# Optimization experiments

Hardware: AMD Instinct MI355X
Metric: run time of the kernel (lower is better)

The kernel has to match this reference:

```python
import jax, jax.numpy as jnp
import numpy as np

DIM = 192
HEADS = 6
HIDDEN = 384  # int(dim * mlp_ratio)


def conv2d(x, w, b=None, padding=0, groups=1):
    out = jax.lax.conv_general_dilated(
        x, w, (1, 1), [(padding, padding), (padding, padding)],
        feature_group_count=groups,
        dimension_numbers=('NCHW', 'OIHW', 'NCHW'))
    return out if b is None else out + b[None, :, None, None]


def layernorm(x, g, b, eps=1e-5):
    m = x.mean(-1, keepdims=True)
    v = x.var(-1, keepdims=True)  # biased, matches torch LayerNorm
    return (x - m) / jnp.sqrt(v + eps) * g + b


def l2norm(x, eps=1e-12):  # F.normalize(dim=-1)
    n = jnp.linalg.norm(x, axis=-1, keepdims=True)
    return x / jnp.maximum(n, eps)


def setup_inputs() -> dict:
    key = jax.random.key(0)
    ks = jax.random.split(key, 12)
    s = 0.02
    return {
        'x': jax.random.normal(ks[0], (4, DIM, 128, 128), dtype=jnp.float32),
        'g1': jnp.ones((DIM,), jnp.float32),
        'b1': jnp.zeros((DIM,), jnp.float32),
        'w_qkv': jax.random.normal(ks[1], (3 * DIM, DIM, 1, 1), jnp.float32) * s,
        'w_dw': jax.random.normal(ks[2], (3 * DIM, 1, 3, 3), jnp.float32) * s,
        'temp': jnp.ones((HEADS, 1, 1), jnp.float32),
        'w_head': jax.random.normal(ks[3], (HEADS, HEADS, 3, 3), jnp.float32) * s,
        'w_proj': jax.random.normal(ks[4], (DIM, DIM, 1, 1), jnp.float32) * s,
        'g2': jnp.ones((DIM,), jnp.float32),
        'b2': jnp.zeros((DIM,), jnp.float32),
        'w_fc1': jax.random.normal(ks[5], (HIDDEN, DIM), jnp.float32) * s,
        'b_fc1': jnp.zeros((HIDDEN,), jnp.float32),
        'w_fc2': jax.random.normal(ks[6], (DIM, HIDDEN), jnp.float32) * s,
        'b_fc2': jnp.zeros((DIM,), jnp.float32),
        'w_sa': jax.random.normal(ks[7], (1, DIM, 3, 3), jnp.float32) * s,
        'b_sa': jnp.zeros((1,), jnp.float32),
    }


def reference(x, g1, b1, w_qkv, w_dw, temp, w_head, w_proj, g2, b2,
              w_fc1, b_fc1, w_fc2, b_fc2, w_sa, b_sa):
    b, c, h, w = x.shape
    hw = h * w
    # norm1 (note: original code re-assigns x, so residual uses normed x)
    xf = x.reshape(b, c, hw).transpose(0, 2, 1)          # [b, hw, c]
    x1 = layernorm(xf, g1, b1).transpose(0, 2, 1).reshape(b, c, h, w)
    # channel attention (Restormer style)
    qkv = conv2d(conv2d(x1, w_qkv), w_dw, padding=1, groups=3 * c)
    q, k, v = jnp.split(qkv, 3, axis=1)
    cp = c // HEADS
    q = l2norm(q.reshape(b, HEADS, cp, hw))
    k = l2norm(k.reshape(b, HEADS, cp, hw))
    v = v.reshape(b, HEADS, cp, hw)
    attn = jnp.einsum('bhcn,bhdn->bhcd', q, k) * temp    # [b, heads, cp, cp]
    attn = conv2d(attn, w_head, padding=1)               # conv over head channels
    attn = jax.nn.softmax(attn, axis=-1)
    out = jnp.einsum('bhcd,bhdn->bhcn', attn, v).reshape(b, c, h, w)
    out = conv2d(out, w_proj)
    x2 = x1 + out
    # MLP branch with spatial-gating attn
    x3 = x2.reshape(b, c, hw).transpose(0, 2, 1)         # [b, hw, c]
    y = layernorm(x3, g2, b2)
    y = jax.nn.gelu(y @ w_fc1.T + b_fc1, approximate=False)
    y = y @ w_fc2.T + b_fc2
    y = jax.nn.gelu(y, approximate=False)                # SAAttn act_fn
    y4 = y.reshape(b, h, w, c).transpose(0, 3, 1, 2)     # [b, c, h, w]
    gate = jax.nn.sigmoid(conv2d(y4, w_sa, b_sa, padding=1))  # [b,1,h,w]
    y = (y4 * gate).reshape(b, c, hw).transpose(0, 2, 1)
    x4 = x3 + y
    return x4.transpose(0, 2, 1).reshape(b, c, h, w)
```

## Files before the change

kernel.cpp:

```cpp
#include <hip/hip_runtime.h>
#include <hip/hip_bf16.h>
#include <math.h>

using bf16 = __hip_bfloat16;

static constexpr int CDIM   = 192;
static constexpr int HEADS  = 6;
static constexpr int CP     = 32;
static constexpr int HIDDEN = 384;
static constexpr int HImg   = 128;
static constexpr int WImg   = 128;
static constexpr int HW     = HImg * WImg;
static constexpr int BATCH  = 4;
static constexpr int PCHUNK = 256;
static constexpr int CSPLIT = 12;

typedef __attribute__((ext_vector_type(8))) short short8;
typedef __attribute__((ext_vector_type(4))) float f32x4;
typedef __attribute__((ext_vector_type(4))) unsigned short ushort4v;
typedef __attribute__((ext_vector_type(8))) unsigned short ushort8v;

template<typename T> __device__ inline float tof(T v);
template<> __device__ inline float tof<float>(float v){ return v; }
template<> __device__ inline float tof<bf16>(bf16 v){ return __bfloat162float(v); }

template<typename T> __device__ inline T fromf(float v);
template<> __device__ inline float fromf<float>(float v){ return v; }
template<> __device__ inline bf16  fromf<bf16>(float v){ return __float2bfloat16(v); }

__device__ inline unsigned short f2bf_bits(float f){
    bf16 h = __float2bfloat16(f);
    return *reinterpret_cast<unsigned short*>(&h);
}
__device__ inline float bfbits2f(unsigned short u){
    union { unsigned int i; float f; } c; c.i = ((unsigned int)u) << 16; return c.f;
}

__device__ inline float gelu_exact(float x){
    return 0.5f * x * (1.0f + erff(x * 0.70710678118654752440f));
}

__device__ inline void load4f(const float* p, float* f){
    f32x4 v = *reinterpret_cast<const f32x4*>(p);
    f[0]=v[0]; f[1]=v[1]; f[2]=v[2]; f[3]=v[3];
}
__device__ inline void load4f(const bf16* p, float* f){
    ushort4v v = *reinterpret_cast<const ushort4v*>(p);
    f[0]=bfbits2f(v[0]); f[1]=bfbits2f(v[1]); f[2]=bfbits2f(v[2]); f[3]=bfbits2f(v[3]);
}

__device__ __forceinline__ void gload16(const bf16* g, bf16* l){
    __builtin_amdgcn_global_load_lds(
        (const __attribute__((address_space(1))) void*)g,
        (__attribute__((address_space(3))) void*)l, 16, 0, 0);
}

__global__ __launch_bounds__(256) void convw_kernel(
    const float* __restrict__ w_qkv, const float* __restrict__ w_proj,
    const float* __restrict__ w_fc1, const float* __restrict__ w_fc2,
    bf16* __restrict__ wq, bf16* __restrict__ wp,
    bf16* __restrict__ wf1, bf16* __restrict__ wf2)
{
    int i = blockIdx.x * 256 + threadIdx.x;
    const int n0 = 576*192, n1 = n0 + 192*192, n2 = n1 + 384*192, n3 = n2 + 192*384;
    if (i < n0)      wq[i]       = fromf<bf16>(w_qkv[i]);
    else if (i < n1) wp[i - n0]  = fromf<bf16>(w_proj[i - n0]);
    else if (i < n2) wf1[i - n1] = fromf<bf16>(w_fc1[i - n1]);
    else if (i < n3) wf2[i - n2] = fromf<bf16>(w_fc2[i - n2]);
}

template<typename T, bool WRES>
__global__ __launch_bounds__(256) void ln_fused_kernel(
    const T* __restrict__ in, const float* __restrict__ g,
    const float* __restrict__ b, bf16* __restrict__ resF, bf16* __restrict__ outT)
{
    int z = blockIdx.y, p0 = blockIdx.x * 64;
    __shared__ float tile[CDIM][65];
    __shared__ float sred[4][64], s2red[4][64];
    __shared__ float mrow[64], rrow[64];
    const T* ib = in + (size_t)z * CDIM * HW + p0;
    int tid = threadIdx.x;
    for (int j = tid; j < CDIM * 16; j += 256){
        int c = j >> 4, p4 = (j & 15) * 4;
        float f[4];
        load4f(ib + (size_t)c * HW + p4, f);
        tile[c][p4]   = f[0]; tile[c][p4+1] = f[1];
        tile[c][p4+2] = f[2]; tile[c][p4+3] = f[3];
    }
    __syncthreads();
    int p = tid & 63, q = tid >> 6;
    float s = 0.f, s2 = 0.f;
    #pragma unroll 4
    for (int c = q * 48; c < q * 48 + 48; ++c){
        float v = tile[c][p]; s += v; s2 += v * v;
    }
    sred[q][p] = s; s2red[q][p] = s2;
    __syncthreads();
    if (tid < 64){
        float ts = sred[0][tid] + sred[1][tid] + sred[2][tid] + sred[3][tid];
        float t2 = s2red[0][tid] + s2red[1][tid] + s2red[2][tid] + s2red[3][tid];
        float mean = ts * (1.0f / CDIM);
        float var  = t2 * (1.0f / CDIM) - mean * mean;
        mrow[tid] = mean;
        rrow[tid] = rsqrtf(var + 1e-5f);
    }
    __syncthreads();
    unsigned short* oT = (unsigned short*)(outT + ((size_t)z * HW + p0) * CDIM);
    for (int j = tid; j < 64 * 48; j += 256){
        int pr = j / 48, c4 = (j % 48) * 4;
        float m = mrow[pr], r = rrow[pr];
        ushort4v o;
        #pragma unroll
        for (int k = 0; k < 4; ++k){
            int c = c4 + k;
            o[k] = f2bf_bits((tile[c][pr] - m) * r * g[c] + b[c]);
        }
        *(ushort4v*)&oT[(size_t)pr * CDIM + c4] = o;
    }
    if (WRES){
        unsigned short* oF = (unsigned short*)resF + (size_t)z * CDIM * HW + p0;
        for (int j = tid; j < CDIM * 16; j += 256){
            int c = j >> 4, p4 = (j & 15) * 4;
            float gg = g[c], bb = b[c];
            ushort4v v;
            #pragma unroll
            for (int k = 0; k < 4; ++k)
                v[k] = f2bf_bits((tile[c][p4 + k] - mrow[p4 + k]) * rrow[p4 + k] * gg + bb);
            *(ushort4v*)&oF[(size_t)c * HW + p4] = v;
        }
    }
}

template<int EPI>
__global__ __launch_bounds__(256) void gemm_mfma_kernel(
    const bf16* __restrict__ Wb, const bf16* __restrict__ XT,
    void* __restrict__ Cout, const float* __restrict__ bias,
    const bf16* __restrict__ res, int M, int K)
{
    __shared__ bf16 smem[40960];
    bf16* Ab0 = smem;
    bf16* Ab1 = smem + 4096;
    bf16* Bb0 = smem + 8192;
    bf16* Bb1 = smem + 8192 + 16384;
    int z  = blockIdx.z;
    int n0 = blockIdx.x * 256;
    int m0 = blockIdx.y * 64;
    const bf16* Xb = XT + (size_t)z * (size_t)HW * K;
    int tid  = threadIdx.x;
    int lane = tid & 63, wid = tid >> 6;
    int r16 = lane & 15, grp = lane >> 4;

    f32x4 acc[4][4];
    #pragma unroll
    for (int i = 0; i < 4; ++i)
        #pragma unroll
        for (int j = 0; j < 4; ++j){ f32x4 zz = {0.f,0.f,0.f,0.f}; acc[i][j] = zz; }

    auto STAGE = [&](int kt, int buf){
        bf16* Al = buf ? Ab1 : Ab0;
        bf16* Bl = buf ? Bb1 : Bb0;
        #pragma unroll
        for (int i = 0; i < 2; ++i){
            int s = i * 256 + tid;
            int row = s >> 3, ch = s & 7;
            gload16(Wb + (size_t)(m0 + row) * K + kt * 64 + ((ch ^ (row & 7)) * 8),
                    Al + s * 8);
        }
        #pragma unroll
        for (int i = 0; i < 8; ++i){
            int s = i * 256 + tid;
            int row = s >> 3, ch = s & 7;
            gload16(Xb + (size_t)(n0 + row) * K + kt * 64 + ((ch ^ (row & 7)) * 8),
                    Bl + s * 8);
        }
    };

    int nkt = K >> 6;
    STAGE(0, 0);
    int cur = 0;
    for (int kt = 0; kt < nkt; ++kt){
        if (kt + 1 < nkt){
            STAGE(kt + 1, cur ^ 1);
            asm volatile("s_waitcnt vmcnt(10)" ::: "memory");
        } else {
            asm volatile("s_waitcnt vmcnt(0)" ::: "memory");
        }
        __builtin_amdgcn_s_barrier();
        bf16* Al = cur ? Ab1 : Ab0;
        bf16* Bl = cur ? Bb1 : Bb0;
        #pragma unroll
        for (int ks = 0; ks < 2; ++ks){
            int kel = ks * 32 + grp * 8;
            short8 a[4], b[4];
            #pragma unroll
            for (int f = 0; f < 4; ++f){
                int arow = f * 16 + r16;
                a[f] = *reinterpret_cast<const short8*>(Al + arow * 64 + (kel ^ ((arow & 7) * 8)));
                int brow = wid * 64 + f * 16 + r16;
                b[f] = *reinterpret_cast<const short8*>(Bl + brow * 64 + (kel ^ ((brow & 7) * 8)));
            }
            #pragma unroll
            for (int fi = 0; fi < 4; ++fi)
                #pragma unroll
                for (int fj = 0; fj < 4; ++fj)
                    acc[fi][fj] = __builtin_amdgcn_mfma_f32_16x16x32_bf16(
                        a[fi], b[fj], acc[fi][fj], 0, 0, 0);
        }
        asm volatile("s_waitcnt lgkmcnt(0)" ::: "memory");
        __builtin_amdgcn_s_barrier();
        cur ^= 1;
    }

    if (EPI == 3){
        unsigned short* T = (unsigned short*)smem;
        #pragma unroll
        for (int fi = 0; fi < 4; ++fi)
            #pragma unroll
            for (int fj = 0; fj < 4; ++fj){
                int nl = wid * 64 + fj * 16 + r16;
                int mb = fi * 16 + grp * 4;
                #pragma unroll
                for (int rr = 0; rr < 4; ++rr){
                    float v = gelu_exact(acc[fi][fj][rr] + bias[m0 + mb + rr]);
                    T[nl * 72 + mb + rr] = f2bf_bits(v);
                }
            }
        asm volatile("s_waitcnt lgkmcnt(0)" ::: "memory");
        __builtin_amdgcn_s_barrier();
        bf16* Y = (bf16*)Cout;
        const short8* srcv = reinterpret_cast<const short8*>(T + tid * 72);
        short8* dstv = reinterpret_cast<short8*>(
            Y + ((size_t)z * HW + n0 + tid) * M + m0);
        #pragma unroll
        for (int i = 0; i < 8; ++i) dstv[i] = srcv[i];
        return;
    }

    {
        unsigned short* T = (unsigned short*)smem;
        #pragma unroll
        for (int fi = 0; fi < 4; ++fi)
            #pragma unroll
            for (int fj = 0; fj < 4; ++fj){
                int m = fi * 16 + grp * 4;
                int n = wid * 64 + fj * 16 + r16;
                #pragma unroll
                for (int rr = 0; rr < 4; ++rr)
                    T[(m + rr) * 264 + n] = f2bf_bits(acc[fi][fj][rr]);
            }
        asm volatile("s_waitcnt lgkmcnt(0)" ::: "memory");
        __builtin_amdgcn_s_barrier();
        int row = tid >> 2, c8 = (tid & 3) * 8;
        bf16* Cb = (bf16*)Cout;
        size_t gbase = (size_t)z * M * HW + (size_t)(m0 + row) * HW + n0 + c8;
        float bv = (EPI == 2) ? bias[m0 + row] : 0.f;
        #pragma unroll
        for (int j = 0; j < 8; ++j){
            int coff = j * 32;
            ushort8v t8 = *(const ushort8v*)&T[row * 264 + c8 + coff];
            ushort8v o8;
            if (EPI == 0){
                o8 = t8;
            } else if (EPI == 1){
                ushort8v r8 = *(const ushort8v*)((const unsigned short*)res + gbase + coff);
                #pragma unroll
                for (int k = 0; k < 8; ++k)
                    o8[k] = f2bf_bits(bfbits2f(t8[k]) + bfbits2f(r8[k]));
            } else {
                #pragma unroll
                for (int k = 0; k < 8; ++k)
                    o8[k] = f2bf_bits(gelu_exact(bfbits2f(t8[k]) + bv));
            }
            *(ushort8v*)((unsigned short*)Cb + gbase + coff) = o8;
        }
    }
}

__global__ __launch_bounds__(256) void dw_kernel(
    const bf16* __restrict__ in, const float* __restrict__ wdw,
    bf16* __restrict__ out, float* __restrict__ sqp)
{
    int ch = blockIdx.y, z = blockIdx.z;
    int tid = threadIdx.x;
    int idx = blockIdx.x * 2048 + tid * 8;
    int yy = idx >> 7, xx = idx & 127;
    const unsigned short* p =
        (const unsigned short*)(in + ((size_t)z * 3 * CDIM + ch) * HW);
    float w[9];
    #pragma unroll
    for (int t = 0; t < 9; ++t) w[t] = wdw[ch * 9 + t];
    float f[3][8], lf[3], rf[3];
    #pragma unroll
    for (int dy = 0; dy < 3; ++dy){
        int iy = yy + dy - 1;
        if (iy >= 0 && iy < HImg){
            ushort8v v8 = *(const ushort8v*)(p + iy * WImg + xx);
            #pragma unroll
            for (int j = 0; j < 8; ++j) f[dy][j] = bfbits2f(v8[j]);
        } else {
            #pragma unroll
            for (int j = 0; j < 8; ++j) f[dy][j] = 0.f;
        }
        float l = __shfl_up(f[dy][7], 1);
        float r = __shfl_down(f[dy][0], 1);
        lf[dy] = (xx == 0) ? 0.f : l;
        rf[dy] = (xx + 8 >= WImg) ? 0.f : r;
    }
    ushort8v o8;
    float sq = 0.f;
    #pragma unroll
    for (int j = 0; j < 8; ++j){
        float a = 0.f;
        #pragma unroll
        for (int dy = 0; dy < 3; ++dy){
            float e0 = (j == 0) ? lf[dy] : f[dy][j - 1];
            float e2 = (j == 7) ? rf[dy] : f[dy][j + 1];
            a = fmaf(w[dy*3], e0, fmaf(w[dy*3+1], f[dy][j], fmaf(w[dy*3+2], e2, a)));
        }
        o8[j] = f2bf_bits(a);
        sq = fmaf(a, a, sq);
    }
    *(ushort8v*)((unsigned short*)(out + ((size_t)z * 3 * CDIM + ch) * HW) + idx) = o8;
    if (ch < 2 * CDIM){
        #pragma unroll
        for (int m = 1; m < 64; m <<= 1) sq += __shfl_xor(sq, m, 64);
        __shared__ float red[4];
        if ((tid & 63) == 0) red[tid >> 6] = sq;
        __syncthreads();
        if (tid == 0)
            sqp[((size_t)ch * BATCH + z) * 8 + blockIdx.x] =
                red[0] + red[1] + red[2] + red[3];
    }
}

__global__ __launch_bounds__(256) void attn_qk_kernel(
    const bf16* __restrict__ qkv, const float* __restrict__ sqp,
    const float* __restrict__ temp, float* __restrict__ part)
{
    int chunk = blockIdx.x;
    int h = blockIdx.y, z = blockIdx.z;
    __shared__ unsigned short qs[CP][PCHUNK + 4];
    __shared__ unsigned short ks[CP][PCHUNK + 4];
    __shared__ float invqs[CP], invks[CP];
    int tid = threadIdx.x;
    if (tid < 2 * CP){
        int which = tid >> 5, cc = tid & 31;
        int ch = which * CDIM + h * CP + cc;
        const float* sp = &sqp[((size_t)ch * BATCH + z) * 8];
        float s = sp[0]+sp[1]+sp[2]+sp[3]+sp[4]+sp[5]+sp[6]+sp[7];
        float inv = 1.0f / fmaxf(sqrtf(s), 1e-12f);
        (which ? invks : invqs)[cc] = inv;
    }
    int n0 = chunk * PCHUNK;
    const unsigned short* qb = (const unsigned short*)(qkv + ((size_t)z * 3 * CDIM + h * CP) * HW);
    const unsigned short* kb = (const unsigned short*)(qkv + ((size_t)z * 3 * CDIM + CDIM + h * CP) * HW);
    for (int i = tid; i < CP * (PCHUNK / 4); i += 256){
        int r = i >> 6, p4 = i & 63;
        *(ushort4v*)&qs[r][p4 * 4] = *(const ushort4v*)&qb[(size_t)r * HW + n0 + p4 * 4];
        *(ushort4v*)&ks[r][p4 * 4] = *(const ushort4v*)&kb[(size_t)r * HW + n0 + p4 * 4];
    }
    __syncthreads();
    int c  = tid >> 3;
    int d0 = (tid & 7) * 4;
    float acc[4] = {0.f, 0.f, 0.f, 0.f};
    for (int p4 = 0; p4 < PCHUNK / 4; ++p4){
        ushort4v qv = *(const ushort4v*)&qs[c][p4 * 4];
        float qf0 = bfbits2f(qv[0]), qf1 = bfbits2f(qv[1]);
        float qf2 = bfbits2f(qv[2]), qf3 = bfbits2f(qv[3]);
        #pragma unroll
        for (int j = 0; j < 4; ++j){
            ushort4v kv = *(const ushort4v*)&ks[d0 + j][p4 * 4];
            acc[j] = fmaf(qf0, bfbits2f(kv[0]),
                     fmaf(qf1, bfbits2f(kv[1]),
                     fmaf(qf2, bfbits2f(kv[2]),
                     fmaf(qf3, bfbits2f(kv[3]), acc[j]))));
        }
    }
    float sc = invqs[c] * temp[h];
    size_t base = ((size_t)chunk * BATCH * HEADS + (size_t)z * HEADS + h) * CP * CP
                + c * CP + d0;
    #pragma unroll
    for (int j = 0; j < 4; ++j)
        part[base + j] = acc[j] * sc * invks[d0 + j];
}

__global__ __launch_bounds__(256) void attn_reduce_kernel(
    const float* __restrict__ part, float* __restrict__ attn)
{
    int idx = blockIdx.x * 256 + threadIdx.x;
    float s = 0.f;
    for (int ch = 0; ch < HW / PCHUNK; ++ch)
        s += part[(size_t)ch * (BATCH * HEADS * CP * CP) + idx];
    attn[idx] = s;
}

__global__ __launch_bounds__(256) void headconv_softmax_kernel(
    const float* __restrict__ attn, const float* __restrict__ wh,
    float* __restrict__ attn2)
{
    int oh = blockIdx.x, z = blockIdx.y;
    __shared__ float wsm[HEADS * 9];
    __shared__ float ain[HEADS][CP * CP];
    __shared__ float aout[CP * CP];
    int tid = threadIdx.x;
    if (tid < HEADS * 9) wsm[tid] = wh[oh * HEADS * 9 + tid];
    for (int i = tid; i < HEADS * CP * CP; i += 256)
        ain[i >> 10][i & 1023] = attn[((size_t)z * HEADS + (i >> 10)) * CP * CP + (i & 1023)];
    __syncthreads();
    for (int idx = tid; idx < CP * CP; idx += 256){
        int i = idx >> 5, j = idx & 31;
        float acc = 0.f;
        #pragma unroll
        for (int ih = 0; ih < HEADS; ++ih){
            #pragma unroll
            for (int dy = 0; dy < 3; ++dy){
                int ii = i + dy - 1;
                if (ii < 0 || ii >= CP) continue;
                #pragma unroll
                for (int dx = 0; dx < 3; ++dx){
                    int jj = j + dx - 1;
                    if (jj < 0 || jj >= CP) continue;
                    acc += wsm[ih * 9 + dy * 3 + dx] * ain[ih][ii * CP + jj];
                }
            }
        }
        aout[idx] = acc;
    }
    __syncthreads();
    int r = tid >> 3, l8 = tid & 7;
    float v[4];
    #pragma unroll
    for (int k = 0; k < 4; ++k) v[k] = aout[r * CP + l8 * 4 + k];
    float mx = fmaxf(fmaxf(v[0], v[1]), fmaxf(v[2], v[3]));
    #pragma unroll
    for (int m = 1; m < 8; m <<= 1) mx = fmaxf(mx, __shfl_xor(mx, m, 64));
    float sum = 0.f;
    #pragma unroll
    for (int k = 0; k < 4; ++k){ v[k] = expf(v[k] - mx); sum += v[k]; }
    #pragma unroll
    for (int m = 1; m < 8; m <<= 1) sum += __shfl_xor(sum, m, 64);
    float rs = 1.0f / sum;
    float* o = attn2 + ((size_t)z * HEADS + oh) * CP * CP + r * CP + l8 * 4;
    #pragma unroll
    for (int k = 0; k < 4; ++k) o[k] = v[k] * rs;
}

__global__ __launch_bounds__(256) void av_kernel(
    const float* __restrict__ attn2, const bf16* __restrict__ qkv, bf16* __restrict__ outT)
{
    int h = blockIdx.y, z = blockIdx.z;
    int tid = threadIdx.x;
    __shared__ float As[CP][CP];
    __shared__ unsigned short Vs[CP][PCHUNK];
    __shared__ unsigned short ot[256][36];
    for (int i = tid; i < CP * CP; i += 256)
        As[i >> 5][i & 31] = attn2[((size_t)(z * HEADS + h)) * CP * CP + i];
    int n0 = blockIdx.x * 256;
    const unsigned short* vb =
        (const unsigned short*)(qkv + ((size_t)z * 3 * CDIM + 2 * CDIM + h * CP) * HW) + n0;
    for (int i = tid; i < CP * 64; i += 256){
        int d = i >> 6, p4 = (i & 63) * 4;
        *(ushort4v*)&Vs[d][p4] = *(const ushort4v*)(vb + (size_t)d * HW + p4);
    }
    __syncthreads();
    float vreg[CP];
    #pragma unroll
    for (int d = 0; d < CP; ++d) vreg[d] = bfbits2f(Vs[d][tid]);
    for (int c = 0; c < CP; ++c){
        float acc = 0.f;
        #pragma unroll
        for (int d = 0; d < CP; ++d) acc = fmaf(As[c][d], vreg[d], acc);
        ot[tid][c] = f2bf_bits(acc);
    }
    __syncthreads();
    unsigned short* ob = (unsigned short*)outT
        + ((size_t)z * HW + (size_t)n0) * CDIM + h * CP;
    for (int j = tid; j < 256 * 8; j += 256){
        int row = j >> 3, q4 = (j & 7) * 4;
        *(ushort4v*)&ob[(size_t)row * CDIM + q4] = *(ushort4v*)&ot[row][q4];
    }
}

__global__ __launch_bounds__(256) void gate_partial_kernel(
    const bf16* __restrict__ y, const float* __restrict__ wsa,
    float* __restrict__ part_g)
{
    int cs = blockIdx.y, z = blockIdx.z;
    __shared__ float wsm[16 * 9];
    if (threadIdx.x < 144) wsm[threadIdx.x] = wsa[cs * 144 + threadIdx.x];
    __syncthreads();
    int idx = blockIdx.x * 2048 + threadIdx.x * 8;
    int yy = idx >> 7, xx = idx & 127;
    const unsigned short* yb =
        (const unsigned short*)(y + (size_t)z * CDIM * HW + (size_t)cs * 16 * HW);
    float acc[8] = {0.f,0.f,0.f,0.f,0.f,0.f,0.f,0.f};
    for (int c = 0; c < 16; ++c){
        const unsigned short* pc = yb + (size_t)c * HW;
        #pragma unroll
        for (int dy = 0; dy < 3; ++dy){
            int iy = yy + dy - 1;
            float f[8], lf, rf;
            if (iy >= 0 && iy < HImg){
                ushort8v v8 = *(const ushort8v*)(pc + iy * WImg + xx);
                #pragma unroll
                for (int j = 0; j < 8; ++j) f[j] = bfbits2f(v8[j]);
            } else {
                #pragma unroll
                for (int j = 0; j < 8; ++j) f[j] = 0.f;
            }
            float l = __shfl_up(f[7], 1);
            float r = __shfl_down(f[0], 1);
            lf = (xx == 0) ? 0.f : l;
            rf = (xx + 8 >= WImg) ? 0.f : r;
            const float* wr = &wsm[c * 9 + dy * 3];
            #pragma unroll
            for (int j = 0; j < 8; ++j){
                float e0 = (j == 0) ? lf : f[j - 1];
                float e2 = (j == 7) ? rf : f[j + 1];
                acc[j] = fmaf(wr[0], e0, fmaf(wr[1], f[j], fmaf(wr[2], e2, acc[j])));
            }
        }
    }
    float* og = &part_g[((size_t)cs * BATCH + z) * HW + idx];
    f32x4 o0 = {acc[0], acc[1], acc[2], acc[3]};
    f32x4 o1 = {acc[4], acc[5], acc[6], acc[7]};
    *(f32x4*)og = o0;
    *(f32x4*)(og + 4) = o1;
}

__global__ __launch_bounds__(256) void gate_finish_kernel(
    const float* __restrict__ part_g, const float* __restrict__ bsa,
    float* __restrict__ gate)
{
    int i4 = (blockIdx.x * 256 + threadIdx.x) * 4;
    float b0 = bsa[0];
    f32x4 acc = {b0, b0, b0, b0};
    #pragma unroll
    for (int cs = 0; cs < CSPLIT; ++cs){
        f32x4 v = *(const f32x4*)&part_g[(size_t)cs * BATCH * HW + i4];
        #pragma unroll
        for (int j = 0; j < 4; ++j) acc[j] += v[j];
    }
    f32x4 o;
    #pragma unroll
    for (int j = 0; j < 4; ++j) o[j] = 1.0f / (1.0f + expf(-acc[j]));
    *(f32x4*)&gate[i4] = o;
}

__global__ __launch_bounds__(256) void final_kernel(
    const bf16* __restrict__ x2, const bf16* __restrict__ y2,
    const float* __restrict__ gate, float* __restrict__ out)
{
    size_t i8 = ((size_t)blockIdx.x * 256 + threadIdx.x) * 8;
    int n = (int)(i8 % HW);
    int z = (int)(i8 / ((size_t)CDIM * HW));
    ushort8v a8 = *(const ushort8v*)((const unsigned short*)x2 + i8);
    ushort8v b8 = *(const ushort8v*)((const unsigned short*)y2 + i8);
    const float* gp = gate + (size_t)z * HW + n;
    f32x4 g0 = *(const f32x4*)gp;
    f32x4 g1 = *(const f32x4*)(gp + 4);
    f32x4 o0, o1;
    #pragma unroll
    for (int j = 0; j < 4; ++j){
        o0[j] = bfbits2f(a8[j])     + bfbits2f(b8[j])     * g0[j];
        o1[j] = bfbits2f(a8[j + 4]) + bfbits2f(b8[j + 4]) * g1[j];
    }
    *(f32x4*)(out + i8) = o0;
    *(f32x4*)(out + i8 + 4) = o1;
}

extern "C" void kernel_launch(void* const* d_in, const int* in_sizes, int n_in,
                              void* d_out, int out_size, void* d_ws, size_t ws_size,
                              hipStream_t stream)
{
    const float* x      = (const float*)d_in[0];
    const float* g1     = (const float*)d_in[1];
    const float* b1     = (const float*)d_in[2];
    const float* w_qkv  = (const float*)d_in[3];
    const float* w_dw   = (const float*)d_in[4];
    const float* temp   = (const float*)d_in[5];
    const float* w_head = (const float*)d_in[6];
    const float* w_proj = (const float*)d_in[7];
    const float* g2     = (const float*)d_in[8];
    const float* b2     = (const float*)d_in[9];
    const float* w_fc1  = (const float*)d_in[10];
    const float* b_fc1  = (const float*)d_in[11];
    const float* w_fc2  = (const float*)d_in[12];
    const float* b_fc2  = (const float*)d_in[13];
    const float* w_sa   = (const float*)d_in[14];
    const float* b_sa   = (const float*)d_in[15];
    float* out = (float*)d_out;

    char* ws = (char*)d_ws;
    const size_t FULL = (size_t)BATCH * CDIM * HW;

    bf16* x1 = (bf16*)ws;
    bf16* y2 = x1;
    char* R1 = ws + FULL * 2;
    bf16*  qkvA      = (bf16*)R1;
    bf16*  attn_outT = (bf16*)R1;
    bf16*  ln2T      = (bf16*)R1;
    bf16*  y1T       = (bf16*)(R1 + FULL * 2);
    char* R2 = R1 + FULL * 3 * 2;
    bf16*  x1T = (bf16*)R2;
    bf16*  dwB = (bf16*)R2;
    bf16*  x2  = (bf16*)R2;
    char* SM = R2 + FULL * 3 * 2;
    float* attn   = (float*)SM;
    float* attn2  = attn + BATCH * HEADS * CP * CP;
    float* gate   = attn2 + BATCH * HEADS * CP * CP;
    float* sqp    = gate + BATCH * HW;
    float* part   = sqp + 2 * CDIM * BATCH * 8;
    float* part_g = part;
    bf16* wq_b  = (bf16*)(part + (HW / PCHUNK) * BATCH * HEADS * CP * CP);
    bf16* wp_b  = wq_b  + 576 * 192;
    bf16* wf1_b = wp_b  + 192 * 192;
    bf16* wf2_b = wf1_b + 384 * 192;

    dim3 blk(256);

    convw_kernel<<<dim3((294912 + 255) / 256), blk, 0, stream>>>(
        w_qkv, w_proj, w_fc1, w_fc2, wq_b, wp_b, wf1_b, wf2_b);
    ln_fused_kernel<float, true><<<dim3(HW / 64, BATCH), blk, 0, stream>>>(
        x, g1, b1, x1, x1T);
    gemm_mfma_kernel<0><<<dim3(HW / 256, (3 * CDIM) / 64, BATCH), blk, 0, stream>>>(
        wq_b, x1T, qkvA, nullptr, nullptr, 3 * CDIM, CDIM);
    dw_kernel<<<dim3(HW / 2048, 3 * CDIM, BATCH), blk, 0, stream>>>(qkvA, w_dw, dwB, sqp);
    attn_qk_kernel<<<dim3(HW / PCHUNK, HEADS, BATCH), blk, 0, stream>>>(
        dwB, sqp, temp, part);
    attn_reduce_kernel<<<dim3((BATCH * HEADS * CP * CP) / 256), blk, 0, stream>>>(part, attn);
    headconv_softmax_kernel<<<dim3(HEADS, BATCH), blk, 0, stream>>>(attn, w_head, attn2);
    av_kernel<<<dim3(HW / 256, HEADS, BATCH), blk, 0, stream>>>(attn2, dwB, attn_outT);
    gemm_mfma_kernel<1><<<dim3(HW / 256, CDIM / 64, BATCH), blk, 0, stream>>>(
        wp_b, attn_outT, x2, nullptr, x1, CDIM, CDIM);
    ln_fused_kernel<bf16, false><<<dim3(HW / 64, BATCH), blk, 0, stream>>>(
        x2, g2, b2, nullptr, ln2T);
    gemm_mfma_kernel<3><<<dim3(HW / 256, HIDDEN / 64, BATCH), blk, 0, stream>>>(
        wf1_b, ln2T, y1T, b_fc1, nullptr, HIDDEN, CDIM);
    gemm_mfma_kernel<2><<<dim3(HW / 256, CDIM / 64, BATCH), blk, 0, stream>>>(
        wf2_b, y1T, y2, b_fc2, nullptr, CDIM, HIDDEN);
    gate_partial_kernel<<<dim3(HW / 2048, CSPLIT, BATCH), blk, 0, stream>>>(
        y2, w_sa, part_g);
    gate_finish_kernel<<<dim3(BATCH * HW / 1024), blk, 0, stream>>>(part_g, b_sa, gate);
    final_kernel<<<dim3((int)(FULL / 2048)), blk, 0, stream>>>(x2, y2, gate, out);
}
```

Baseline: 315.3 us.

## Load MFMA GEMM fragments directly from global memory instead of LDS staging

The GEMM kernel drops its double-buffered global-to-LDS staging pipeline, with its swizzle and barriers. Each wave now reads its A and B MFMA fragments straight from global memory. K becomes a template parameter so the K loop is fully unrolled, and shared memory is cut to only the epilogue transpose buffer. The aim is to remove LDS round-trips and per-tile barriers, and to raise occupancy through lower LDS use. The cost is narrower, less coalesced global loads (64-byte row segments), A fragments reread by every wave, and possibly high register pressure from the unrolled loads.

```diff
diff --git a/kernel.cpp b/kernel.cpp
--- a/kernel.cpp
+++ b/kernel.cpp
@@ -47,12 +47,6 @@
 __device__ inline void load4f(const bf16* p, float* f){
     ushort4v v = *reinterpret_cast<const ushort4v*>(p);
     f[0]=bfbits2f(v[0]); f[1]=bfbits2f(v[1]); f[2]=bfbits2f(v[2]); f[3]=bfbits2f(v[3]);
-}
-
-__device__ __forceinline__ void gload16(const bf16* g, bf16* l){
-    __builtin_amdgcn_global_load_lds(
-        (const __attribute__((address_space(1))) void*)g,
-        (__attribute__((address_space(3))) void*)l, 16, 0, 0);
 }
 
 __global__ __launch_bounds__(256) void convw_kernel(
@@ -131,88 +125,47 @@
     }
 }
 
-template<int EPI>
+template<int EPI, int KT>
 __global__ __launch_bounds__(256) void gemm_mfma_kernel(
     const bf16* __restrict__ Wb, const bf16* __restrict__ XT,
     void* __restrict__ Cout, const float* __restrict__ bias,
-    const bf16* __restrict__ res, int M, int K)
-{
-    __shared__ bf16 smem[40960];
-    bf16* Ab0 = smem;
-    bf16* Ab1 = smem + 4096;
-    bf16* Bb0 = smem + 8192;
-    bf16* Bb1 = smem + 8192 + 16384;
+    const bf16* __restrict__ res, int M)
+{
+    __shared__ unsigned short T[256 * 72];
     int z  = blockIdx.z;
     int n0 = blockIdx.x * 256;
     int m0 = blockIdx.y * 64;
-    const bf16* Xb = XT + (size_t)z * (size_t)HW * K;
+    const bf16* Xb = XT + (size_t)z * (size_t)HW * KT;
     int tid  = threadIdx.x;
     int lane = tid & 63, wid = tid >> 6;
     int r16 = lane & 15, grp = lane >> 4;
 
+    const bf16* Ap = Wb + (size_t)(m0 + r16) * KT + grp * 8;
+    const bf16* Bp = Xb + (size_t)(n0 + wid * 64 + r16) * KT + grp * 8;
+
     f32x4 acc[4][4];
     #pragma unroll
     for (int i = 0; i < 4; ++i)
         #pragma unroll
         for (int j = 0; j < 4; ++j){ f32x4 zz = {0.f,0.f,0.f,0.f}; acc[i][j] = zz; }
 
-    auto STAGE = [&](int kt, int buf){
-        bf16* Al = buf ? Ab1 : Ab0;
-        bf16* Bl = buf ? Bb1 : Bb0;
-        #pragma unroll
-        for (int i = 0; i < 2; ++i){
-            int s = i * 256 + tid;
-            int row = s >> 3, ch = s & 7;
-            gload16(Wb + (size_t)(m0 + row) * K + kt * 64 + ((ch ^ (row & 7)) * 8),
-                    Al + s * 8);
-        }
-        #pragma unroll
-        for (int i = 0; i < 8; ++i){
-            int s = i * 256 + tid;
-            int row = s >> 3, ch = s & 7;
-            gload16(Xb + (size_t)(n0 + row) * K + kt * 64 + ((ch ^ (row & 7)) * 8),
-                    Bl + s * 8);
-        }
-    };
-
-    int nkt = K >> 6;
-    STAGE(0, 0);
-    int cur = 0;
-    for (int kt = 0; kt < nkt; ++kt){
-        if (kt + 1 < nkt){
-            STAGE(kt + 1, cur ^ 1);
-            asm volatile("s_waitcnt vmcnt(10)" ::: "memory");
-        } else {
-            asm volatile("s_waitcnt vmcnt(0)" ::: "memory");
-        }
-        __builtin_amdgcn_s_barrier();
-        bf16* Al = cur ? Ab1 : Ab0;
-        bf16* Bl = cur ? Bb1 : Bb0;
-        #pragma unroll
-        for (int ks = 0; ks < 2; ++ks){
-            int kel = ks * 32 + grp * 8;
-            short8 a[4], b[4];
-            #pragma unroll
-            for (int f = 0; f < 4; ++f){
-                int arow = f * 16 + r16;
-                a[f] = *reinterpret_cast<const short8*>(Al + arow * 64 + (kel ^ ((arow & 7) * 8)));
-                int brow = wid * 64 + f * 16 + r16;
-                b[f] = *reinterpret_cast<const short8*>(Bl + brow * 64 + (kel ^ ((brow & 7) * 8)));
-            }
-            #pragma unroll
-            for (int fi = 0; fi < 4; ++fi)
-                #pragma unroll
-                for (int fj = 0; fj < 4; ++fj)
-                    acc[fi][fj] = __builtin_amdgcn_mfma_f32_16x16x32_bf16(
-                        a[fi], b[fj], acc[fi][fj], 0, 0, 0);
-        }
-        asm volatile("s_waitcnt lgkmcnt(0)" ::: "memory");
-        __builtin_amdgcn_s_barrier();
-        cur ^= 1;
+    #pragma unroll
+    for (int kk = 0; kk < KT / 32; ++kk){
+        short8 a[4], b[4];
+        #pragma unroll
+        for (int f = 0; f < 4; ++f){
+            a[f] = *reinterpret_cast<const short8*>(Ap + (size_t)f * 16 * KT + kk * 32);
+            b[f] = *reinterpret_cast<const short8*>(Bp + (size_t)f * 16 * KT + kk * 32);
+        }
+        #pragma unroll
+        for (int fi = 0; fi < 4; ++fi)
+            #pragma unroll
+            for (int fj = 0; fj < 4; ++fj)
+                acc[fi][fj] = __builtin_amdgcn_mfma_f32_16x16x32_bf16(
+                    a[fi], b[fj], acc[fi][fj], 0, 0, 0);
     }
 
     if (EPI == 3){
-        unsigned short* T = (unsigned short*)smem;
         #pragma unroll
         for (int fi = 0; fi < 4; ++fi)
             #pragma unroll
@@ -236,43 +189,40 @@
         return;
     }
 
-    {
-        unsigned short* T = (unsigned short*)smem;
-        #pragma unroll
-        for (int fi = 0; fi < 4; ++fi)
-            #pragma unroll
-            for (int fj = 0; fj < 4; ++fj){
-                int m = fi * 16 + grp * 4;
-                int n = wid * 64 + fj * 16 + r16;
-                #pragma unroll
-                for (int rr = 0; rr < 4; ++rr)
-                    T[(m + rr) * 264 + n] = f2bf_bits(acc[fi][fj][rr]);
-            }
-        asm volatile("s_waitcnt lgkmcnt(0)" ::: "memory");
-        __builtin_amdgcn_s_barrier();
-        int row = tid >> 2, c8 = (tid & 3) * 8;
-        bf16* Cb = (bf16*)Cout;
-        size_t gbase = (size_t)z * M * HW + (size_t)(m0 + row) * HW + n0 + c8;
-        float bv = (EPI == 2) ? bias[m0 + row] : 0.f;
-        #pragma unroll
-        for (int j = 0; j < 8; ++j){
-            int coff = j * 32;
-            ushort8v t8 = *(const ushort8v*)&T[row * 264 + c8 + coff];
-            ushort8v o8;
-            if (EPI == 0){
-                o8 = t8;
-            } else if (EPI == 1){
-                ushort8v r8 = *(const ushort8v*)((const unsigned short*)res + gbase + coff);
-                #pragma unroll
-                for (int k = 0; k < 8; ++k)
-                    o8[k] = f2bf_bits(bfbits2f(t8[k]) + bfbits2f(r8[k]));
-            } else {
-                #pragma unroll
-                for (int k = 0; k < 8; ++k)
-                    o8[k] = f2bf_bits(gelu_exact(bfbits2f(t8[k]) + bv));
-            }
-            *(ushort8v*)((unsigned short*)Cb + gbase + coff) = o8;
-        }
+    #pragma unroll
+    for (int fi = 0; fi < 4; ++fi)
+        #pragma unroll
+        for (int fj = 0; fj < 4; ++fj){
+            int m = fi * 16 + grp * 4;
+            int n = wid * 64 + fj * 16 + r16;
+            #pragma unroll
+            for (int rr = 0; rr < 4; ++rr)
+                T[(m + rr) * 264 + n] = f2bf_bits(acc[fi][fj][rr]);
+        }
+    asm volatile("s_waitcnt lgkmcnt(0)" ::: "memory");
+    __builtin_amdgcn_s_barrier();
+    int row = tid >> 2, c8 = (tid & 3) * 8;
+    bf16* Cb = (bf16*)Cout;
+    size_t gbase = (size_t)z * M * HW + (size_t)(m0 + row) * HW + n0 + c8;
+    float bv = (EPI == 2) ? bias[m0 + row] : 0.f;
+    #pragma unroll
+    for (int j = 0; j < 8; ++j){
+        int coff = j * 32;
+        ushort8v t8 = *(const ushort8v*)&T[row * 264 + c8 + coff];
+        ushort8v o8;
+        if (EPI == 0){
+            o8 = t8;
+        } else if (EPI == 1){
+            ushort8v r8 = *(const ushort8v*)((const unsigned short*)res + gbase + coff);
+            #pragma unroll
+            for (int k = 0; k < 8; ++k)
+                o8[k] = f2bf_bits(bfbits2f(t8[k]) + bfbits2f(r8[k]));
+        } else {
+            #pragma unroll
+            for (int k = 0; k < 8; ++k)
+                o8[k] = f2bf_bits(gelu_exact(bfbits2f(t8[k]) + bv));
+        }
+        *(ushort8v*)((unsigned short*)Cb + gbase + coff) = o8;
     }
 }
 
@@ -623,22 +573,22 @@
         w_qkv, w_proj, w_fc1, w_fc2, wq_b, wp_b, wf1_b, wf2_b);
     ln_fused_kernel<float, true><<<dim3(HW / 64, BATCH), blk, 0, stream>>>(
         x, g1, b1, x1, x1T);
-    gemm_mfma_kernel<0><<<dim3(HW / 256, (3 * CDIM) / 64, BATCH), blk, 0, stream>>>(
-        wq_b, x1T, qkvA, nullptr, nullptr, 3 * CDIM, CDIM);
+    gemm_mfma_kernel<0, 192><<<dim3(HW / 256, (3 * CDIM) / 64, BATCH), blk, 0, stream>>>(
+        wq_b, x1T, qkvA, nullptr, nullptr, 3 * CDIM);
     dw_kernel<<<dim3(HW / 2048, 3 * CDIM, BATCH), blk, 0, stream>>>(qkvA, w_dw, dwB, sqp);
     attn_qk_kernel<<<dim3(HW / PCHUNK, HEADS, BATCH), blk, 0, stream>>>(
         dwB, sqp, temp, part);
     attn_reduce_kernel<<<dim3((BATCH * HEADS * CP * CP) / 256), blk, 0, stream>>>(part, attn);
     headconv_softmax_kernel<<<dim3(HEADS, BATCH), blk, 0, stream>>>(attn, w_head, attn2);
     av_kernel<<<dim3(HW / 256, HEADS, BATCH), blk, 0, stream>>>(attn2, dwB, attn_outT);
-    gemm_mfma_kernel<1><<<dim3(HW / 256, CDIM / 64, BATCH), blk, 0, stream>>>(
-        wp_b, attn_outT, x2, nullptr, x1, CDIM, CDIM);
+    gemm_mfma_kernel<1, 192><<<dim3(HW / 256, CDIM / 64, BATCH), blk, 0, stream>>>(
+        wp_b, attn_outT, x2, nullptr, x1, CDIM);
     ln_fused_kernel<bf16, false><<<dim3(HW / 64, BATCH), blk, 0, stream>>>(
         x2, g2, b2, nullptr, ln2T);
-    gemm_mfma_kernel<3><<<dim3(HW / 256, HIDDEN / 64, BATCH), blk, 0, stream>>>(
-        wf1_b, ln2T, y1T, b_fc1, nullptr, HIDDEN, CDIM);
-    gemm_mfma_kernel<2><<<dim3(HW / 256, CDIM / 64, BATCH), blk, 0, stream>>>(
-        wf2_b, y1T, y2, b_fc2, nullptr, CDIM, HIDDEN);
+    gemm_mfma_kernel<3, 192><<<dim3(HW / 256, HIDDEN / 64, BATCH), blk, 0, stream>>>(
+        wf1_b, ln2T, y1T, b_fc1, nullptr, HIDDEN);
+    gemm_mfma_kernel<2, 384><<<dim3(HW / 256, CDIM / 64, BATCH), blk, 0, stream>>>(
+        wf2_b, y1T, y2, b_fc2, nullptr, CDIM);
     gate_partial_kernel<<<dim3(HW / 2048, CSPLIT, BATCH), blk, 0, stream>>>(
         y2, w_sa, part_g);
     gate_finish_kernel<<<dim3(BATCH * HW / 1024), blk, 0, stream>>>(part_g, b_sa, gate);
```

Result: slower. 371.7 us (+17.9%).

## Single-buffer GEMM LDS staging and compute two rows per thread in depthwise conv

Applied to the files above, without the earlier changes.

The MFMA GEMM drops its double-buffered LDS prefetch in favour of a single buffer with a full wait and barrier per k-tile. This halves shared memory per block, possibly raising occupancy, but loses load/compute overlap. The depthwise 3x3 conv now has each thread produce two output rows from four loaded rows, reducing redundant row loads. It also halves the grid and the number of sum-of-squares partials consumed by the attention kernel.

```diff
diff --git a/kernel.cpp b/kernel.cpp
--- a/kernel.cpp
+++ b/kernel.cpp
@@ -14,6 +14,7 @@
 static constexpr int BATCH  = 4;
 static constexpr int PCHUNK = 256;
 static constexpr int CSPLIT = 12;
+static constexpr int DWCHUNK = 4;
 
 typedef __attribute__((ext_vector_type(8))) short short8;
 typedef __attribute__((ext_vector_type(4))) float f32x4;
@@ -137,11 +138,9 @@
     void* __restrict__ Cout, const float* __restrict__ bias,
     const bf16* __restrict__ res, int M, int K)
 {
-    __shared__ bf16 smem[40960];
-    bf16* Ab0 = smem;
-    bf16* Ab1 = smem + 4096;
-    bf16* Bb0 = smem + 8192;
-    bf16* Bb1 = smem + 8192 + 16384;
+    __shared__ bf16 smem[20480];
+    bf16* Als = smem;
+    bf16* Bls = smem + 4096;
     int z  = blockIdx.z;
     int n0 = blockIdx.x * 256;
     int m0 = blockIdx.y * 64;
@@ -156,38 +155,24 @@
         #pragma unroll
         for (int j = 0; j < 4; ++j){ f32x4 zz = {0.f,0.f,0.f,0.f}; acc[i][j] = zz; }
 
-    auto STAGE = [&](int kt, int buf){
-        bf16* Al = buf ? Ab1 : Ab0;
-        bf16* Bl = buf ? Bb1 : Bb0;
+    int nkt = K >> 6;
+    for (int kt = 0; kt < nkt; ++kt){
         #pragma unroll
         for (int i = 0; i < 2; ++i){
             int s = i * 256 + tid;
             int row = s >> 3, ch = s & 7;
             gload16(Wb + (size_t)(m0 + row) * K + kt * 64 + ((ch ^ (row & 7)) * 8),
-                    Al + s * 8);
+                    Als + s * 8);
         }
         #pragma unroll
         for (int i = 0; i < 8; ++i){
             int s = i * 256 + tid;
             int row = s >> 3, ch = s & 7;
             gload16(Xb + (size_t)(n0 + row) * K + kt * 64 + ((ch ^ (row & 7)) * 8),
-                    Bl + s * 8);
-        }
-    };
-
-    int nkt = K >> 6;
-    STAGE(0, 0);
-    int cur = 0;
-    for (int kt = 0; kt < nkt; ++kt){
-        if (kt + 1 < nkt){
-            STAGE(kt + 1, cur ^ 1);
-            asm volatile("s_waitcnt vmcnt(10)" ::: "memory");
-        } else {
-            asm volatile("s_waitcnt vmcnt(0)" ::: "memory");
-        }
-        __builtin_amdgcn_s_barrier();
-        bf16* Al = cur ? Ab1 : Ab0;
-        bf16* Bl = cur ? Bb1 : Bb0;
+                    Bls + s * 8);
+        }
+        asm volatile("s_waitcnt vmcnt(0)" ::: "memory");
+        __syncthreads();
         #pragma unroll
         for (int ks = 0; ks < 2; ++ks){
             int kel = ks * 32 + grp * 8;
@@ -195,9 +180,9 @@
             #pragma unroll
             for (int f = 0; f < 4; ++f){
                 int arow = f * 16 + r16;
-                a[f] = *reinterpret_cast<const short8*>(Al + arow * 64 + (kel ^ ((arow & 7) * 8)));
+                a[f] = *reinterpret_cast<const short8*>(Als + arow * 64 + (kel ^ ((arow & 7) * 8)));
                 int brow = wid * 64 + f * 16 + r16;
-                b[f] = *reinterpret_cast<const short8*>(Bl + brow * 64 + (kel ^ ((brow & 7) * 8)));
+                b[f] = *reinterpret_cast<const short8*>(Bls + brow * 64 + (kel ^ ((brow & 7) * 8)));
             }
             #pragma unroll
             for (int fi = 0; fi < 4; ++fi)
@@ -206,9 +191,7 @@
                     acc[fi][fj] = __builtin_amdgcn_mfma_f32_16x16x32_bf16(
                         a[fi], b[fj], acc[fi][fj], 0, 0, 0);
         }
-        asm volatile("s_waitcnt lgkmcnt(0)" ::: "memory");
-        __builtin_amdgcn_s_barrier();
-        cur ^= 1;
+        __syncthreads();
     }
 
     if (EPI == 3){
@@ -225,8 +208,7 @@
                     T[nl * 72 + mb + rr] = f2bf_bits(v);
                 }
             }
-        asm volatile("s_waitcnt lgkmcnt(0)" ::: "memory");
-        __builtin_amdgcn_s_barrier();
+        __syncthreads();
         bf16* Y = (bf16*)Cout;
         const short8* srcv = reinterpret_cast<const short8*>(T + tid * 72);
         short8* dstv = reinterpret_cast<short8*>(
@@ -248,8 +230,7 @@
                 for (int rr = 0; rr < 4; ++rr)
                     T[(m + rr) * 264 + n] = f2bf_bits(acc[fi][fj][rr]);
             }
-        asm volatile("s_waitcnt lgkmcnt(0)" ::: "memory");
-        __builtin_amdgcn_s_barrier();
+        __syncthreads();
         int row = tid >> 2, c8 = (tid & 3) * 8;
         bf16* Cb = (bf16*)Cout;
         size_t gbase = (size_t)z * M * HW + (size_t)(m0 + row) * HW + n0 + c8;
@@ -282,45 +263,51 @@
 {
     int ch = blockIdx.y, z = blockIdx.z;
     int tid = threadIdx.x;
-    int idx = blockIdx.x * 2048 + tid * 8;
-    int yy = idx >> 7, xx = idx & 127;
+    int rp = tid >> 4;
+    int xx = (tid & 15) * 8;
+    int y0 = blockIdx.x * 32 + rp * 2;
     const unsigned short* p =
         (const unsigned short*)(in + ((size_t)z * 3 * CDIM + ch) * HW);
     float w[9];
     #pragma unroll
     for (int t = 0; t < 9; ++t) w[t] = wdw[ch * 9 + t];
-    float f[3][8], lf[3], rf[3];
-    #pragma unroll
-    for (int dy = 0; dy < 3; ++dy){
-        int iy = yy + dy - 1;
+    float f[4][8], lf[4], rf[4];
+    #pragma unroll
+    for (int r = 0; r < 4; ++r){
+        int iy = y0 - 1 + r;
         if (iy >= 0 && iy < HImg){
             ushort8v v8 = *(const ushort8v*)(p + iy * WImg + xx);
             #pragma unroll
-            for (int j = 0; j < 8; ++j) f[dy][j] = bfbits2f(v8[j]);
+            for (int j = 0; j < 8; ++j) f[r][j] = bfbits2f(v8[j]);
         } else {
             #pragma unroll
-            for (int j = 0; j < 8; ++j) f[dy][j] = 0.f;
-        }
-        float l = __shfl_up(f[dy][7], 1);
-        float r = __shfl_down(f[dy][0], 1);
-        lf[dy] = (xx == 0) ? 0.f : l;
-        rf[dy] = (xx + 8 >= WImg) ? 0.f : r;
-    }
-    ushort8v o8;
+            for (int j = 0; j < 8; ++j) f[r][j] = 0.f;
+        }
+        float l = __shfl_up(f[r][7], 1);
+        float rr_ = __shfl_down(f[r][0], 1);
+        lf[r] = (xx == 0) ? 0.f : l;
+        rf[r] = (xx + 8 >= WImg) ? 0.f : rr_;
+    }
     float sq = 0.f;
-    #pragma unroll
-    for (int j = 0; j < 8; ++j){
-        float a = 0.f;
-        #pragma unroll
-        for (int dy = 0; dy < 3; ++dy){
-            float e0 = (j == 0) ? lf[dy] : f[dy][j - 1];
-            float e2 = (j == 7) ? rf[dy] : f[dy][j + 1];
-            a = fmaf(w[dy*3], e0, fmaf(w[dy*3+1], f[dy][j], fmaf(w[dy*3+2], e2, a)));
-        }
-        o8[j] = f2bf_bits(a);
-        sq = fmaf(a, a, sq);
-    }
-    *(ushort8v*)((unsigned short*)(out + ((size_t)z * 3 * CDIM + ch) * HW) + idx) = o8;
+    unsigned short* ob = (unsigned short*)(out + ((size_t)z * 3 * CDIM + ch) * HW);
+    #pragma unroll
+    for (int orow = 0; orow < 2; ++orow){
+        ushort8v o8;
+        #pragma unroll
+        for (int j = 0; j < 8; ++j){
+            float a = 0.f;
+            #pragma unroll
+            for (int dy = 0; dy < 3; ++dy){
+                int r = orow + dy;
+                float e0 = (j == 0) ? lf[r] : f[r][j - 1];
+                float e2 = (j == 7) ? rf[r] : f[r][j + 1];
+                a = fmaf(w[dy*3], e0, fmaf(w[dy*3+1], f[r][j], fmaf(w[dy*3+2], e2, a)));
+            }
+            o8[j] = f2bf_bits(a);
+            sq = fmaf(a, a, sq);
+        }
+        *(ushort8v*)(ob + (y0 + orow) * WImg + xx) = o8;
+    }
     if (ch < 2 * CDIM){
         #pragma unroll
         for (int m = 1; m < 64; m <<= 1) sq += __shfl_xor(sq, m, 64);
@@ -328,7 +315,7 @@
         if ((tid & 63) == 0) red[tid >> 6] = sq;
         __syncthreads();
         if (tid == 0)
-            sqp[((size_t)ch * BATCH + z) * 8 + blockIdx.x] =
+            sqp[((size_t)ch * BATCH + z) * DWCHUNK + blockIdx.x] =
                 red[0] + red[1] + red[2] + red[3];
     }
 }
@@ -346,8 +333,8 @@
     if (tid < 2 * CP){
         int which = tid >> 5, cc = tid & 31;
         int ch = which * CDIM + h * CP + cc;
-        const float* sp = &sqp[((size_t)ch * BATCH + z) * 8];
-        float s = sp[0]+sp[1]+sp[2]+sp[3]+sp[4]+sp[5]+sp[6]+sp[7];
+        const float* sp = &sqp[((size_t)ch * BATCH + z) * DWCHUNK];
+        float s = sp[0] + sp[1] + sp[2] + sp[3];
         float inv = 1.0f / fmaxf(sqrtf(s), 1e-12f);
         (which ? invks : invqs)[cc] = inv;
     }
@@ -610,7 +597,7 @@
     float* attn2  = attn + BATCH * HEADS * CP * CP;
     float* gate   = attn2 + BATCH * HEADS * CP * CP;
     float* sqp    = gate + BATCH * HW;
-    float* part   = sqp + 2 * CDIM * BATCH * 8;
+    float* part   = sqp + 2 * CDIM * BATCH * DWCHUNK;
     float* part_g = part;
     bf16* wq_b  = (bf16*)(part + (HW / PCHUNK) * BATCH * HEADS * CP * CP);
     bf16* wp_b  = wq_b  + 576 * 192;
@@ -625,7 +612,7 @@
         x, g1, b1, x1, x1T);
     gemm_mfma_kernel<0><<<dim3(HW / 256, (3 * CDIM) / 64, BATCH), blk, 0, stream>>>(
         wq_b, x1T, qkvA, nullptr, nullptr, 3 * CDIM, CDIM);
-    dw_kernel<<<dim3(HW / 2048, 3 * CDIM, BATCH), blk, 0, stream>>>(qkvA, w_dw, dwB, sqp);
+    dw_kernel<<<dim3(DWCHUNK, 3 * CDIM, BATCH), blk, 0, stream>>>(qkvA, w_dw, dwB, sqp);
     attn_qk_kernel<<<dim3(HW / PCHUNK, HEADS, BATCH), blk, 0, stream>>>(
         dwB, sqp, temp, part);
     attn_reduce_kernel<<<dim3((BATCH * HEADS * CP * CP) / 256), blk, 0, stream>>>(part, attn);
```

After: 297.2 us. -5.7%, faster.
